# Kernel optimization log

Hardware: AMD Instinct MI355X
Metric: run time of the kernel (lower is better)

Reference implementation:

```python
import jax, jax.numpy as jnp
import numpy as np

B, D, W = 2048, 512, 512
DEPTH = 6
N_BINS = 2 ** DEPTH          # 64 leaves
N_NODES = 2 ** DEPTH - 1     # 63 inner nodes


def build_indices(depth: int) -> np.ndarray:
    """Root-to-leaf path index table into hstack([probs, 1-probs]).
    Index j selects probs[:, j]; index j + N selects 1 - probs[:, j]."""
    n = 2 ** depth - 1
    paths = []
    for b in range(2 ** depth):
        node, path = 0, []
        for level in range(depth):
            bit = (b >> (depth - 1 - level)) & 1
            path.append(node if bit == 0 else node + n)
            node = 2 * node + 1 + bit
        paths.append(path)
    return np.asarray(paths, dtype=np.int32)  # [2**depth, depth]


def setup_inputs() -> dict:
    key = jax.random.key(0)
    k1, k2, k3, k4 = jax.random.split(key, 4)
    x = jax.random.normal(k1, (B, D), dtype=jnp.float32)
    ray = jax.random.normal(k2, (1, D), dtype=jnp.float32)  # kaiming-normal init
    w_i = jnp.zeros((1, N_NODES), dtype=jnp.float32)
    b_i = jax.random.normal(k3, (1, N_NODES), dtype=jnp.float32)
    a_i = 5.0 * jnp.ones((1, N_NODES), dtype=jnp.float32)
    # kaiming-normal over fan_in = input_width
    inner_transforms = jax.random.normal(k4, (N_BINS, D, W), dtype=jnp.float32) * np.float32((2.0 / D) ** 0.5)
    idx = jnp.asarray(build_indices(DEPTH))  # [64, 6] int32
    return {"x": x, "ray": ray, "w_i": w_i, "b_i": b_i, "a_i": a_i,
            "inner_transforms": inner_transforms, "idx": idx}


def reference(x, ray, w_i, b_i, a_i, inner_transforms, idx):
    eps = 1e-8
    # angles: arccos(cosine_similarity(x, ray)) / pi  -> [B]
    xn = jnp.maximum(jnp.linalg.norm(x, axis=1), eps)
    rn = jnp.maximum(jnp.linalg.norm(ray, axis=1), eps)  # [1]
    cos = (x @ ray[0]) / (xn * rn)
    angles = jnp.arccos(cos) / jnp.pi  # [B]
    # per-node decision probabilities: [B, N_NODES]
    node_fns = (0.5 + jax.nn.sigmoid(w_i)) * angles[:, None] - jax.nn.sigmoid(b_i)
    decisions = jax.nn.sigmoid(node_fns * (1.0 + a_i))
    # tree-indexed gather + product over path -> soft bin distribution [B, N_BINS]
    stacked = jnp.concatenate([decisions, 1.0 - decisions], axis=1)  # [B, 2N]
    bins, depth = idx.shape
    gathered = stacked[:, idx.reshape(-1)].reshape(x.shape[0], bins, depth)
    distribution = jnp.prod(gathered, axis=2)  # [B, L]
    # per-bin linear transforms, weighted by the distribution
    inner = jnp.einsum('bi,liw->blw', x, inner_transforms)  # [B, L, W]
    return jnp.einsum('bl,blo->bo', distribution, inner)  # [B, W]
```

## Files before the change

### kernel.cpp

```cpp
#include <hip/hip_runtime.h>
#include <math.h>

typedef float  f32x4  __attribute__((ext_vector_type(4)));
typedef short  bf16x8 __attribute__((ext_vector_type(8)));
typedef unsigned short u16x8 __attribute__((ext_vector_type(8)));

#define B_ROWS 2048
#define D_DIM  512
#define W_DIM  512
#define N_NODES 63
#define N_BINS  64
#define K_TOT   32768

__device__ __forceinline__ unsigned short f2bf(float f) {
    union { float f; unsigned int u; } v; v.f = f;
    unsigned int u = v.u;
    return (unsigned short)((u + 0x7fffu + ((u >> 16) & 1u)) >> 16);
}

__device__ __forceinline__ float sigmoidf_(float z) {
    return 1.0f / (1.0f + expf(-z));
}

__global__ __launch_bounds__(256) void k_dist(
    const float* __restrict__ x, const float* __restrict__ ray,
    const float* __restrict__ w_i, const float* __restrict__ b_i,
    const float* __restrict__ a_i, const int* __restrict__ idx,
    float* __restrict__ dist)
{
    const int wid  = threadIdx.x >> 6;
    const int lane = threadIdx.x & 63;
    const int row  = blockIdx.x * 4 + wid;
    const float* xr = x + (size_t)row * D_DIM;

    float dotv = 0.f, xx = 0.f, rr = 0.f;
#pragma unroll
    for (int j = 0; j < 2; ++j) {
        f32x4 xv = *(const f32x4*)(xr  + j * 256 + lane * 4);
        f32x4 rv = *(const f32x4*)(ray + j * 256 + lane * 4);
        dotv += xv.x * rv.x + xv.y * rv.y + xv.z * rv.z + xv.w * rv.w;
        xx   += xv.x * xv.x + xv.y * xv.y + xv.z * xv.z + xv.w * xv.w;
        rr   += rv.x * rv.x + rv.y * rv.y + rv.z * rv.z + rv.w * rv.w;
    }
#pragma unroll
    for (int off = 1; off < 64; off <<= 1) {
        dotv += __shfl_xor(dotv, off, 64);
        xx   += __shfl_xor(xx,   off, 64);
        rr   += __shfl_xor(rr,   off, 64);
    }
    float xn = fmaxf(sqrtf(xx), 1e-8f);
    float rn = fmaxf(sqrtf(rr), 1e-8f);
    float cosv = dotv / (xn * rn);
    cosv = fminf(1.f, fmaxf(-1.f, cosv));
    float angle = acosf(cosv) * 0.31830988618379067f;

    float dec = 0.f;
    if (lane < N_NODES) {
        float sw = sigmoidf_(w_i[lane]);
        float sb = sigmoidf_(b_i[lane]);
        float nf = (0.5f + sw) * angle - sb;
        dec = sigmoidf_(nf * (1.0f + a_i[lane]));
    }

    float p = 1.f;
#pragma unroll
    for (int v = 0; v < 6; ++v) {
        int j = idx[lane * 6 + v];
        int node = (j < N_NODES) ? j : j - N_NODES;
        float d = __shfl(dec, node, 64);
        p *= (j < N_NODES) ? d : (1.0f - d);
    }
    dist[(size_t)row * N_BINS + lane] = p;
}

__global__ __launch_bounds__(256) void k_transpose(
    const float* __restrict__ T, unsigned short* __restrict__ Tt)
{
    __shared__ float tile[32][33];
    const int l  = blockIdx.z;
    const int i0 = blockIdx.x * 32, w0 = blockIdx.y * 32;
    const int tx = threadIdx.x & 31, ty = threadIdx.x >> 5;
    const float* src = T + ((size_t)(l * 512 + i0)) * 512 + w0;
#pragma unroll
    for (int r = 0; r < 4; ++r) {
        int i = ty + r * 8;
        tile[i][tx] = src[(size_t)i * 512 + tx];
    }
    __syncthreads();
    unsigned short* dst = Tt + (size_t)w0 * K_TOT + l * 512 + i0;
#pragma unroll
    for (int r = 0; r < 4; ++r) {
        int w = ty + r * 8;
        dst[(size_t)w * K_TOT + tx] = f2bf(tile[tx][w]);
    }
}

__global__ __launch_bounds__(256, 2) void k_gemm_bt(
    const float* __restrict__ x, const float* __restrict__ dist,
    const unsigned short* __restrict__ Tt, float* __restrict__ part,
    int kchunk)
{
    __shared__ unsigned short As[128][72];
    __shared__ unsigned short Bs[128][64];

    const int bm0 = blockIdx.x * 128;
    const int bn0 = blockIdx.y * 128;
    const int kbase = blockIdx.z * kchunk;

    const int lane = threadIdx.x & 63;
    const int wid  = threadIdx.x >> 6;
    const int wm = wid >> 1, wn = wid & 1;
    const int lq = lane >> 4, lr = lane & 15;

    f32x4 acc[4][4];
#pragma unroll
    for (int a = 0; a < 4; ++a)
#pragma unroll
        for (int b = 0; b < 4; ++b)
            acc[a][b] = (f32x4){0.f, 0.f, 0.f, 0.f};

    const int iters = kchunk / 64;
    for (int it = 0; it < iters; ++it) {
        const int k0 = kbase + it * 64;
        const int l  = k0 >> 9;
        const int i0 = k0 & 511;

#pragma unroll
        for (int r2 = 0; r2 < 8; ++r2) {
            int id = threadIdx.x + r2 * 256;
            int m  = id >> 4;
            int kc = id & 15;
            float sc = dist[(size_t)(bm0 + m) * N_BINS + l];
            f32x4 v = *(const f32x4*)(x + (size_t)(bm0 + m) * D_DIM + i0 + kc * 4);
            v *= sc;
            unsigned int p0 = (unsigned int)f2bf(v.x) | ((unsigned int)f2bf(v.y) << 16);
            unsigned int p1 = (unsigned int)f2bf(v.z) | ((unsigned int)f2bf(v.w) << 16);
            unsigned int* dp = (unsigned int*)&As[m][kc * 4];
            dp[0] = p0; dp[1] = p1;
        }
#pragma unroll
        for (int r2 = 0; r2 < 4; ++r2) {
            int id = threadIdx.x + r2 * 256;
            int n  = id >> 3;
            int c  = id & 7;
            int cg = c ^ (n & 7);
            const u16x8 v = *(const u16x8*)(Tt + (size_t)(bn0 + n) * K_TOT + k0 + cg * 8);
            *(u16x8*)&Bs[n][c * 8] = v;
        }
        __syncthreads();

#pragma unroll
        for (int ks = 0; ks < 2; ++ks) {
            bf16x8 af[4], bfr[4];
#pragma unroll
            for (int fm = 0; fm < 4; ++fm)
                af[fm] = *(const bf16x8*)&As[wm * 64 + fm * 16 + lr][ks * 32 + lq * 8];
#pragma unroll
            for (int fn = 0; fn < 4; ++fn) {
                int nl = wn * 64 + fn * 16 + lr;
                int cs = (ks * 4 + lq) ^ (nl & 7);
                bfr[fn] = *(const bf16x8*)&Bs[nl][cs * 8];
            }
#pragma unroll
            for (int fm = 0; fm < 4; ++fm)
#pragma unroll
                for (int fn = 0; fn < 4; ++fn)
                    acc[fm][fn] = __builtin_amdgcn_mfma_f32_16x16x32_bf16(
                        af[fm], bfr[fn], acc[fm][fn], 0, 0, 0);
        }
        __syncthreads();
    }

    float* Cp = part + (size_t)blockIdx.z * (B_ROWS * W_DIM);
#pragma unroll
    for (int fm = 0; fm < 4; ++fm)
#pragma unroll
        for (int fn = 0; fn < 4; ++fn)
#pragma unroll
            for (int r = 0; r < 4; ++r) {
                int row = bm0 + wm * 64 + fm * 16 + lq * 4 + r;
                int col = bn0 + wn * 64 + fn * 16 + lr;
                Cp[(size_t)row * W_DIM + col] = acc[fm][fn][r];
            }
}

__global__ __launch_bounds__(256) void k_reduce(
    const float* __restrict__ part, float* __restrict__ out, int nsplit)
{
    int i = (blockIdx.x * 256 + threadIdx.x) * 4;
    f32x4 s = *(const f32x4*)(part + i);
    for (int p = 1; p < nsplit; ++p)
        s += *(const f32x4*)(part + (size_t)p * (B_ROWS * W_DIM) + i);
    *(f32x4*)(out + i) = s;
}

__global__ __launch_bounds__(256, 2) void k_gemm_fb(
    const float* __restrict__ x, const float* __restrict__ dist,
    const float* __restrict__ T, float* __restrict__ out)
{
    __shared__ unsigned short As[128][72];
    __shared__ unsigned short Bs[128][72];

    const int bm0 = blockIdx.x * 128;
    const int bn0 = blockIdx.y * 128;
    const int lane = threadIdx.x & 63;
    const int wid  = threadIdx.x >> 6;
    const int wm = wid >> 1, wn = wid & 1;
    const int lq = lane >> 4, lr = lane & 15;

    f32x4 acc[4][4];
#pragma unroll
    for (int a = 0; a < 4; ++a)
#pragma unroll
        for (int b = 0; b < 4; ++b)
            acc[a][b] = (f32x4){0.f, 0.f, 0.f, 0.f};

    for (int it = 0; it < K_TOT / 64; ++it) {
        const int k0 = it * 64;
        const int l  = k0 >> 9;
        const int i0 = k0 & 511;
#pragma unroll
        for (int r2 = 0; r2 < 8; ++r2) {
            int id = threadIdx.x + r2 * 256;
            int m  = id >> 4;
            int kc = id & 15;
            float sc = dist[(size_t)(bm0 + m) * N_BINS + l];
            f32x4 v = *(const f32x4*)(x + (size_t)(bm0 + m) * D_DIM + i0 + kc * 4);
            v *= sc;
            unsigned int p0 = (unsigned int)f2bf(v.x) | ((unsigned int)f2bf(v.y) << 16);
            unsigned int p1 = (unsigned int)f2bf(v.z) | ((unsigned int)f2bf(v.w) << 16);
            unsigned int* dp = (unsigned int*)&As[m][kc * 4];
            dp[0] = p0; dp[1] = p1;
        }
#pragma unroll
        for (int r2 = 0; r2 < 8; ++r2) {
            int id = threadIdx.x + r2 * 256;
            int k  = id >> 5;
            int n4 = (id & 31) * 4;
            f32x4 v = *(const f32x4*)(T + ((size_t)(l * 512 + i0 + k)) * 512 + bn0 + n4);
            Bs[n4 + 0][k] = f2bf(v.x);
            Bs[n4 + 1][k] = f2bf(v.y);
            Bs[n4 + 2][k] = f2bf(v.z);
            Bs[n4 + 3][k] = f2bf(v.w);
        }
        __syncthreads();
#pragma unroll
        for (int ks = 0; ks < 2; ++ks) {
            bf16x8 af[4], bfr[4];
#pragma unroll
            for (int fm = 0; fm < 4; ++fm)
                af[fm] = *(const bf16x8*)&As[wm * 64 + fm * 16 + lr][ks * 32 + lq * 8];
#pragma unroll
            for (int fn = 0; fn < 4; ++fn)
                bfr[fn] = *(const bf16x8*)&Bs[wn * 64 + fn * 16 + lr][ks * 32 + lq * 8];
#pragma unroll
            for (int fm = 0; fm < 4; ++fm)
#pragma unroll
                for (int fn = 0; fn < 4; ++fn)
                    acc[fm][fn] = __builtin_amdgcn_mfma_f32_16x16x32_bf16(
                        af[fm], bfr[fn], acc[fm][fn], 0, 0, 0);
        }
        __syncthreads();
    }
#pragma unroll
    for (int fm = 0; fm < 4; ++fm)
#pragma unroll
        for (int fn = 0; fn < 4; ++fn)
#pragma unroll
            for (int r = 0; r < 4; ++r) {
                int row = bm0 + wm * 64 + fm * 16 + lq * 4 + r;
                int col = bn0 + wn * 64 + fn * 16 + lr;
                out[(size_t)row * W_DIM + col] = acc[fm][fn][r];
            }
}

extern "C" void kernel_launch(void* const* d_in, const int* in_sizes, int n_in,
                              void* d_out, int out_size, void* d_ws, size_t ws_size,
                              hipStream_t stream) {
    const float* x   = (const float*)d_in[0];
    const float* ray = (const float*)d_in[1];
    const float* w_i = (const float*)d_in[2];
    const float* b_i = (const float*)d_in[3];
    const float* a_i = (const float*)d_in[4];
    const float* T   = (const float*)d_in[5];
    const int*   idx = (const int*)d_in[6];
    float* out = (float*)d_out;

    char* ws = (char*)d_ws;
    const size_t distBytes = (size_t)B_ROWS * N_BINS * 4;
    const size_t ttBytes   = (size_t)W_DIM * K_TOT * 2;
    const size_t partBytes = (size_t)B_ROWS * W_DIM * 4;

    float* dist = (float*)ws;
    k_dist<<<B_ROWS / 4, 256, 0, stream>>>(x, ray, w_i, b_i, a_i, idx, dist);

    if (ws_size >= distBytes + ttBytes) {
        unsigned short* Tt = (unsigned short*)(ws + distBytes);
        size_t avail = ws_size - distBytes - ttBytes;
        int nsplit = (int)(avail / partBytes);
        if (nsplit > 8) nsplit = 8;
        if (nsplit < 1) nsplit = 1;
        while (nsplit & (nsplit - 1)) --nsplit;

        k_transpose<<<dim3(16, 16, 64), 256, 0, stream>>>(T, Tt);

        float* part = (nsplit > 1) ? (float*)(ws + distBytes + ttBytes) : out;
        k_gemm_bt<<<dim3(16, 4, nsplit), 256, 0, stream>>>(
            x, dist, Tt, part, K_TOT / nsplit);
        if (nsplit > 1)
            k_reduce<<<(B_ROWS * W_DIM) / (256 * 4), 256, 0, stream>>>(part, out, nsplit);
    } else {
        k_gemm_fb<<<dim3(16, 4), 256, 0, stream>>>(x, dist, T, out);
    }
}
```

Baseline: 230.9 us.

## Pre-scale A into bf16 workspace and stream GEMM tiles via global_load_lds

Adds a k_scale pass that materializes the distribution-scaled x as a bf16 [B, 32768] matrix. A new GEMM kernel then loads both A and the transposed T tiles straight into LDS with global_load_lds, using an XOR swizzle, and runs at higher occupancy with up to 16 K-splits. The transpose kernel now uses 64x64 tiles and vectorized 16-byte stores. The cost is a 128 MB extra write and re-read of A, plus a larger workspace. If the workspace is too small it falls back to the old path, and the final fallback kernel is removed.

```diff
diff --git a/kernel.cpp b/kernel.cpp
--- a/kernel.cpp
+++ b/kernel.cpp
@@ -22,6 +22,13 @@
     return 1.0f / (1.0f + expf(-z));
 }
 
+__device__ __forceinline__ void load_lds16(const void* g, void* l) {
+    __builtin_amdgcn_global_load_lds(
+        (const __attribute__((address_space(1))) unsigned int*)g,
+        (__attribute__((address_space(3))) unsigned int*)l,
+        16, 0, 0);
+}
+
 __global__ __launch_bounds__(256) void k_dist(
     const float* __restrict__ x, const float* __restrict__ ray,
     const float* __restrict__ w_i, const float* __restrict__ b_i,
@@ -73,26 +80,143 @@
     dist[(size_t)row * N_BINS + lane] = p;
 }
 
-__global__ __launch_bounds__(256) void k_transpose(
+__global__ __launch_bounds__(256) void k_scale(
+    const float* __restrict__ x, const float* __restrict__ dist,
+    unsigned short* __restrict__ Ap)
+{
+    const int gid = blockIdx.x * 256 + threadIdx.x;
+    const int b  = gid >> 12;
+    const int k8 = gid & 4095;
+    const int k  = k8 * 8;
+    const int l  = k >> 9;
+    const int i  = k & 511;
+    const float sc = dist[b * N_BINS + l];
+    f32x4 v0 = *(const f32x4*)(x + (size_t)b * D_DIM + i);
+    f32x4 v1 = *(const f32x4*)(x + (size_t)b * D_DIM + i + 4);
+    v0 *= sc; v1 *= sc;
+    u16x8 o;
+    o[0] = f2bf(v0.x); o[1] = f2bf(v0.y); o[2] = f2bf(v0.z); o[3] = f2bf(v0.w);
+    o[4] = f2bf(v1.x); o[5] = f2bf(v1.y); o[6] = f2bf(v1.z); o[7] = f2bf(v1.w);
+    *(u16x8*)(Ap + (size_t)gid * 8) = o;
+}
+
+__global__ __launch_bounds__(256) void k_transpose2(
     const float* __restrict__ T, unsigned short* __restrict__ Tt)
 {
-    __shared__ float tile[32][33];
+    __shared__ float tile[64][65];
     const int l  = blockIdx.z;
-    const int i0 = blockIdx.x * 32, w0 = blockIdx.y * 32;
-    const int tx = threadIdx.x & 31, ty = threadIdx.x >> 5;
+    const int i0 = blockIdx.x * 64, w0 = blockIdx.y * 64;
+    const int t  = threadIdx.x;
+
+    const int w4 = (t & 15) * 4;
+    const int ir = t >> 4;
     const float* src = T + ((size_t)(l * 512 + i0)) * 512 + w0;
 #pragma unroll
-    for (int r = 0; r < 4; ++r) {
-        int i = ty + r * 8;
-        tile[i][tx] = src[(size_t)i * 512 + tx];
+    for (int p = 0; p < 4; ++p) {
+        int i = ir + p * 16;
+        f32x4 v = *(const f32x4*)(src + (size_t)i * 512 + w4);
+        tile[i][w4 + 0] = v.x; tile[i][w4 + 1] = v.y;
+        tile[i][w4 + 2] = v.z; tile[i][w4 + 3] = v.w;
     }
     __syncthreads();
-    unsigned short* dst = Tt + (size_t)w0 * K_TOT + l * 512 + i0;
-#pragma unroll
-    for (int r = 0; r < 4; ++r) {
-        int w = ty + r * 8;
-        dst[(size_t)w * K_TOT + tx] = f2bf(tile[tx][w]);
-    }
+#pragma unroll
+    for (int rep = 0; rep < 2; ++rep) {
+        int id = t + rep * 256;
+        int w  = id >> 3;
+        int c  = id & 7;
+        u16x8 o;
+#pragma unroll
+        for (int j = 0; j < 8; ++j) o[j] = f2bf(tile[c * 8 + j][w]);
+        *(u16x8*)(Tt + (size_t)(w0 + w) * K_TOT + l * 512 + i0 + c * 8) = o;
+    }
+}
+
+__global__ __launch_bounds__(256, 4) void k_gemm2(
+    const unsigned short* __restrict__ Ap, const unsigned short* __restrict__ Tt,
+    float* __restrict__ part, int kchunk)
+{
+    __shared__ unsigned short As[128 * 64];
+    __shared__ unsigned short Bs[128 * 64];
+
+    const int bm0 = blockIdx.x * 128;
+    const int bn0 = blockIdx.y * 128;
+    const int kbase = blockIdx.z * kchunk;
+
+    const int t    = threadIdx.x;
+    const int lane = t & 63;
+    const int wid  = t >> 6;
+    const int wm = wid >> 1, wn = wid & 1;
+    const int lq = lane >> 4, lr = lane & 15;
+
+    const int srow = t >> 3;
+    const int c    = t & 7;
+
+    f32x4 acc[4][4];
+#pragma unroll
+    for (int a = 0; a < 4; ++a)
+#pragma unroll
+        for (int b = 0; b < 4; ++b)
+            acc[a][b] = (f32x4){0.f, 0.f, 0.f, 0.f};
+
+    const int iters = kchunk / 64;
+    for (int it = 0; it < iters; ++it) {
+        const int k0 = kbase + it * 64;
+#pragma unroll
+        for (int j = 0; j < 4; ++j) {
+            int row = srow + j * 32;
+            int cg  = c ^ (row & 7);
+            load_lds16(Ap + (size_t)(bm0 + row) * K_TOT + k0 + cg * 8,
+                       &As[row * 64 + c * 8]);
+            load_lds16(Tt + (size_t)(bn0 + row) * K_TOT + k0 + cg * 8,
+                       &Bs[row * 64 + c * 8]);
+        }
+        __syncthreads();
+#pragma unroll
+        for (int ks = 0; ks < 2; ++ks) {
+            bf16x8 af[4], bfr[4];
+#pragma unroll
+            for (int fm = 0; fm < 4; ++fm) {
+                int m = wm * 64 + fm * 16 + lr;
+                int g = ks * 4 + lq;
+                af[fm] = *(const bf16x8*)&As[m * 64 + ((g ^ (m & 7)) * 8)];
+            }
+#pragma unroll
+            for (int fn = 0; fn < 4; ++fn) {
+                int n = wn * 64 + fn * 16 + lr;
+                int g = ks * 4 + lq;
+                bfr[fn] = *(const bf16x8*)&Bs[n * 64 + ((g ^ (n & 7)) * 8)];
+            }
+#pragma unroll
+            for (int fm = 0; fm < 4; ++fm)
+#pragma unroll
+                for (int fn = 0; fn < 4; ++fn)
+                    acc[fm][fn] = __builtin_amdgcn_mfma_f32_16x16x32_bf16(
+                        af[fm], bfr[fn], acc[fm][fn], 0, 0, 0);
+        }
+        __syncthreads();
+    }
+
+    float* Cp = part + (size_t)blockIdx.z * (B_ROWS * W_DIM);
+#pragma unroll
+    for (int fm = 0; fm < 4; ++fm)
+#pragma unroll
+        for (int fn = 0; fn < 4; ++fn)
+#pragma unroll
+            for (int r = 0; r < 4; ++r) {
+                int row = bm0 + wm * 64 + fm * 16 + lq * 4 + r;
+                int col = bn0 + wn * 64 + fn * 16 + lr;
+                Cp[(size_t)row * W_DIM + col] = acc[fm][fn][r];
+            }
+}
+
+__global__ __launch_bounds__(256) void k_reduce(
+    const float* __restrict__ part, float* __restrict__ out, int nsplit)
+{
+    int i = (blockIdx.x * 256 + threadIdx.x) * 4;
+    f32x4 s = *(const f32x4*)(part + i);
+    for (int p = 1; p < nsplit; ++p)
+        s += *(const f32x4*)(part + (size_t)p * (B_ROWS * W_DIM) + i);
+    *(f32x4*)(out + i) = s;
 }
 
 __global__ __launch_bounds__(256, 2) void k_gemm_bt(
@@ -124,7 +248,6 @@
         const int k0 = kbase + it * 64;
         const int l  = k0 >> 9;
         const int i0 = k0 & 511;
-
 #pragma unroll
         for (int r2 = 0; r2 < 8; ++r2) {
             int id = threadIdx.x + r2 * 256;
@@ -142,13 +265,12 @@
         for (int r2 = 0; r2 < 4; ++r2) {
             int id = threadIdx.x + r2 * 256;
             int n  = id >> 3;
-            int c  = id & 7;
-            int cg = c ^ (n & 7);
+            int cc = id & 7;
+            int cg = cc ^ (n & 7);
             const u16x8 v = *(const u16x8*)(Tt + (size_t)(bn0 + n) * K_TOT + k0 + cg * 8);
-            *(u16x8*)&Bs[n][c * 8] = v;
+            *(u16x8*)&Bs[n][cc * 8] = v;
         }
         __syncthreads();
-
 #pragma unroll
         for (int ks = 0; ks < 2; ++ks) {
             bf16x8 af[4], bfr[4];
@@ -181,96 +303,6 @@
                 int row = bm0 + wm * 64 + fm * 16 + lq * 4 + r;
                 int col = bn0 + wn * 64 + fn * 16 + lr;
                 Cp[(size_t)row * W_DIM + col] = acc[fm][fn][r];
-            }
-}
-
-__global__ __launch_bounds__(256) void k_reduce(
-    const float* __restrict__ part, float* __restrict__ out, int nsplit)
-{
-    int i = (blockIdx.x * 256 + threadIdx.x) * 4;
-    f32x4 s = *(const f32x4*)(part + i);
-    for (int p = 1; p < nsplit; ++p)
-        s += *(const f32x4*)(part + (size_t)p * (B_ROWS * W_DIM) + i);
-    *(f32x4*)(out + i) = s;
-}
-
-__global__ __launch_bounds__(256, 2) void k_gemm_fb(
-    const float* __restrict__ x, const float* __restrict__ dist,
-    const float* __restrict__ T, float* __restrict__ out)
-{
-    __shared__ unsigned short As[128][72];
-    __shared__ unsigned short Bs[128][72];
-
-    const int bm0 = blockIdx.x * 128;
-    const int bn0 = blockIdx.y * 128;
-    const int lane = threadIdx.x & 63;
-    const int wid  = threadIdx.x >> 6;
-    const int wm = wid >> 1, wn = wid & 1;
-    const int lq = lane >> 4, lr = lane & 15;
-
-    f32x4 acc[4][4];
-#pragma unroll
-    for (int a = 0; a < 4; ++a)
-#pragma unroll
-        for (int b = 0; b < 4; ++b)
-            acc[a][b] = (f32x4){0.f, 0.f, 0.f, 0.f};
-
-    for (int it = 0; it < K_TOT / 64; ++it) {
-        const int k0 = it * 64;
-        const int l  = k0 >> 9;
-        const int i0 = k0 & 511;
-#pragma unroll
-        for (int r2 = 0; r2 < 8; ++r2) {
-            int id = threadIdx.x + r2 * 256;
-            int m  = id >> 4;
-            int kc = id & 15;
-            float sc = dist[(size_t)(bm0 + m) * N_BINS + l];
-            f32x4 v = *(const f32x4*)(x + (size_t)(bm0 + m) * D_DIM + i0 + kc * 4);
-            v *= sc;
-            unsigned int p0 = (unsigned int)f2bf(v.x) | ((unsigned int)f2bf(v.y) << 16);
-            unsigned int p1 = (unsigned int)f2bf(v.z) | ((unsigned int)f2bf(v.w) << 16);
-            unsigned int* dp = (unsigned int*)&As[m][kc * 4];
-            dp[0] = p0; dp[1] = p1;
-        }
-#pragma unroll
-        for (int r2 = 0; r2 < 8; ++r2) {
-            int id = threadIdx.x + r2 * 256;
-            int k  = id >> 5;
-            int n4 = (id & 31) * 4;
-            f32x4 v = *(const f32x4*)(T + ((size_t)(l * 512 + i0 + k)) * 512 + bn0 + n4);
-            Bs[n4 + 0][k] = f2bf(v.x);
-            Bs[n4 + 1][k] = f2bf(v.y);
-            Bs[n4 + 2][k] = f2bf(v.z);
-            Bs[n4 + 3][k] = f2bf(v.w);
-        }
-        __syncthreads();
-#pragma unroll
-        for (int ks = 0; ks < 2; ++ks) {
-            bf16x8 af[4], bfr[4];
-#pragma unroll
-            for (int fm = 0; fm < 4; ++fm)
-                af[fm] = *(const bf16x8*)&As[wm * 64 + fm * 16 + lr][ks * 32 + lq * 8];
-#pragma unroll
-            for (int fn = 0; fn < 4; ++fn)
-                bfr[fn] = *(const bf16x8*)&Bs[wn * 64 + fn * 16 + lr][ks * 32 + lq * 8];
-#pragma unroll
-            for (int fm = 0; fm < 4; ++fm)
-#pragma unroll
-                for (int fn = 0; fn < 4; ++fn)
-                    acc[fm][fn] = __builtin_amdgcn_mfma_f32_16x16x32_bf16(
-                        af[fm], bfr[fn], acc[fm][fn], 0, 0, 0);
-        }
-        __syncthreads();
-    }
-#pragma unroll
-    for (int fm = 0; fm < 4; ++fm)
-#pragma unroll
-        for (int fn = 0; fn < 4; ++fn)
-#pragma unroll
-            for (int r = 0; r < 4; ++r) {
-                int row = bm0 + wm * 64 + fm * 16 + lq * 4 + r;
-                int col = bn0 + wn * 64 + fn * 16 + lr;
-                out[(size_t)row * W_DIM + col] = acc[fm][fn][r];
             }
 }
 
@@ -288,13 +320,30 @@
 
     char* ws = (char*)d_ws;
     const size_t distBytes = (size_t)B_ROWS * N_BINS * 4;
+    const size_t apBytes   = (size_t)B_ROWS * K_TOT * 2;
     const size_t ttBytes   = (size_t)W_DIM * K_TOT * 2;
     const size_t partBytes = (size_t)B_ROWS * W_DIM * 4;
 
     float* dist = (float*)ws;
     k_dist<<<B_ROWS / 4, 256, 0, stream>>>(x, ray, w_i, b_i, a_i, idx, dist);
 
-    if (ws_size >= distBytes + ttBytes) {
+    if (ws_size >= distBytes + apBytes + ttBytes) {
+        unsigned short* Ap = (unsigned short*)(ws + distBytes);
+        unsigned short* Tt = (unsigned short*)(ws + distBytes + apBytes);
+        size_t avail = ws_size - distBytes - apBytes - ttBytes;
+        int nsplit = (int)(avail / partBytes);
+        if (nsplit > 16) nsplit = 16;
+        if (nsplit < 1) nsplit = 1;
+        while (nsplit & (nsplit - 1)) --nsplit;
+
+        k_scale<<<(B_ROWS * K_TOT / 8) / 256, 256, 0, stream>>>(x, dist, Ap);
+        k_transpose2<<<dim3(8, 8, 64), 256, 0, stream>>>(T, Tt);
+
+        float* part = (nsplit > 1) ? (float*)(ws + distBytes + apBytes + ttBytes) : out;
+        k_gemm2<<<dim3(16, 4, nsplit), 256, 0, stream>>>(Ap, Tt, part, K_TOT / nsplit);
+        if (nsplit > 1)
+            k_reduce<<<(B_ROWS * W_DIM) / (256 * 4), 256, 0, stream>>>(part, out, nsplit);
+    } else if (ws_size >= distBytes + ttBytes) {
         unsigned short* Tt = (unsigned short*)(ws + distBytes);
         size_t avail = ws_size - distBytes - ttBytes;
         int nsplit = (int)(avail / partBytes);
@@ -302,14 +351,11 @@
         if (nsplit < 1) nsplit = 1;
         while (nsplit & (nsplit - 1)) --nsplit;
 
-        k_transpose<<<dim3(16, 16, 64), 256, 0, stream>>>(T, Tt);
-
+        k_transpose2<<<dim3(8, 8, 64), 256, 0, stream>>>(T, Tt);
         float* part = (nsplit > 1) ? (float*)(ws + distBytes + ttBytes) : out;
         k_gemm_bt<<<dim3(16, 4, nsplit), 256, 0, stream>>>(
             x, dist, Tt, part, K_TOT / nsplit);
         if (nsplit > 1)
             k_reduce<<<(B_ROWS * W_DIM) / (256 * 4), 256, 0, stream>>>(part, out, nsplit);
-    } else {
-        k_gemm_fb<<<dim3(16, 4), 256, 0, stream>>>(x, dist, T, out);
-    }
-}
+    }
+}
```

After: 270.3 us. 17.1% more time.
